# Performance work log

Measured on AMD Instinct MI355X. Metric: run time of the kernel, lower is better.

The kernel has to match this reference:

```python
import jax, jax.numpy as jnp
import numpy as np

NUM_EXPERTS = 64
TOP_K = 2


def setup_inputs() -> dict:
    key = jax.random.key(0)
    k1, k2 = jax.random.split(key)
    hidden_states = jax.random.normal(k1, (4, 8192, 2048), dtype=jnp.float32)
    # torch nn.Linear weight layout: (num_experts, hidden)
    W = jax.random.normal(k2, (NUM_EXPERTS, 2048), dtype=jnp.float32) * 0.02
    return {"hidden_states": hidden_states, "W": W}


def reference(hidden_states, W):
    b, s, h = hidden_states.shape
    x = hidden_states.reshape(-1, h)                      # (T, H), T = b*s
    logits = jnp.einsum('th,eh->te', x, W)                # (T, E) skinny gate GEMM
    # eval mode: no gaussian noise added
    top_vals, indices = jax.lax.top_k(logits, TOP_K)      # (T, K)
    gates = jax.nn.softmax(top_vals, axis=-1)
    gates = gates.reshape(b, s, TOP_K)
    indices = indices.reshape(b, s, TOP_K)
    # load-balance auxiliary loss (faithful to source, incl. probs>0 mask)
    probs = jax.nn.softmax(logits, axis=-1)               # (T, E)
    mean_probs = probs.mean(axis=0)                       # (E,)
    routing_probs = (probs > 0).astype(logits.dtype).mean(axis=0)  # (E,)
    load_balance_loss = NUM_EXPERTS * jnp.sum(mean_probs * routing_probs)
    return (gates, indices, load_balance_loss)
```

## Files before the change

kernel.cpp:

```cpp
#include <hip/hip_runtime.h>
#include <math.h>

#define H      2048
#define HV     512
#define E      64
#define MTOK   8
#define T_TOK  32768
#define GATES_OFF   0
#define IDX_OFF     65536
#define LOSS_OFF    131072

__global__ void transpose_w_kernel(const float* __restrict__ W, float* __restrict__ Wt) {
    int id = blockIdx.x * 256 + threadIdx.x;
    int e = id >> 11;
    int h = id & 2047;
    Wt[(h >> 2) * 256 + (e << 2) + (h & 3)] = W[id];
}

__global__ __launch_bounds__(256) void gate_main_kernel(
        const float* __restrict__ x,
        const float4* __restrict__ wt,
        float* __restrict__ out,
        float* __restrict__ accum)
{
    const int lane = threadIdx.x & 63;
    const int wave = threadIdx.x >> 6;
    const int gwave = blockIdx.x * 4 + wave;
    const int tokBase = __builtin_amdgcn_readfirstlane(gwave * MTOK);

    const float4* __restrict__ xq = (const float4*)x + (size_t)tokBase * HV;

    float acc[MTOK];
#pragma unroll
    for (int m = 0; m < MTOK; ++m) acc[m] = 0.f;

    for (int i = 0; i < HV; ++i) {
        float4 wv = wt[i * E + lane];
#pragma unroll
        for (int m = 0; m < MTOK; ++m) {
            float4 xv = xq[m * HV + i];
            acc[m] = fmaf(xv.x, wv.x, acc[m]);
            acc[m] = fmaf(xv.y, wv.y, acc[m]);
            acc[m] = fmaf(xv.z, wv.z, acc[m]);
            acc[m] = fmaf(xv.w, wv.w, acc[m]);
        }
    }

    float sumP = 0.f, cntP = 0.f;

#pragma unroll
    for (int m = 0; m < MTOK; ++m) {
        float v = acc[m];

        float vmax = v;
#pragma unroll
        for (int d = 32; d > 0; d >>= 1) vmax = fmaxf(vmax, __shfl_xor(vmax, d, 64));
        float ex = expf(v - vmax);
        float s = ex;
#pragma unroll
        for (int d = 32; d > 0; d >>= 1) s += __shfl_xor(s, d, 64);
        float p = ex / s;
        sumP += p;
        cntP += (p > 0.f) ? 1.f : 0.f;

        float v1 = v; int i1 = lane;
#pragma unroll
        for (int d = 32; d > 0; d >>= 1) {
            float ov = __shfl_xor(v1, d, 64);
            int   oi = __shfl_xor(i1, d, 64);
            if (ov > v1 || (ov == v1 && oi < i1)) { v1 = ov; i1 = oi; }
        }
        float v2 = (lane == i1) ? -INFINITY : v; int i2 = lane;
#pragma unroll
        for (int d = 32; d > 0; d >>= 1) {
            float ov = __shfl_xor(v2, d, 64);
            int   oi = __shfl_xor(i2, d, 64);
            if (ov > v2 || (ov == v2 && oi < i2)) { v2 = ov; i2 = oi; }
        }

        if (lane == 0) {
            int token = tokBase + m;
            float t  = expf(v2 - v1);
            float d  = 1.f / (1.f + t);
            out[GATES_OFF + 2 * token]     = d;
            out[GATES_OFF + 2 * token + 1] = t * d;
            out[IDX_OFF   + 2 * token]     = (float)i1;
            out[IDX_OFF   + 2 * token + 1] = (float)i2;
        }
    }

    __shared__ float redP[4][64];
    __shared__ float redC[4][64];
    redP[wave][lane] = sumP;
    redC[wave][lane] = cntP;
    __syncthreads();
    if (wave == 0) {
        float sp = redP[0][lane] + redP[1][lane] + redP[2][lane] + redP[3][lane];
        float sc = redC[0][lane] + redC[1][lane] + redC[2][lane] + redC[3][lane];
        atomicAdd(&accum[lane], sp);
        atomicAdd(&accum[E + lane], sc);
    }
}

__global__ void gate_final_kernel(const float* __restrict__ accum, float* __restrict__ out) {
    int lane = threadIdx.x;
    const float invT = 1.f / (float)T_TOK;
    float mean_p   = accum[lane] * invT;
    float routing  = accum[E + lane] * invT;
    float term = mean_p * routing;
#pragma unroll
    for (int d = 32; d > 0; d >>= 1) term += __shfl_xor(term, d, 64);
    if (lane == 0) out[LOSS_OFF] = 64.f * term;
}

extern "C" void kernel_launch(void* const* d_in, const int* in_sizes, int n_in,
                              void* d_out, int out_size, void* d_ws, size_t ws_size,
                              hipStream_t stream) {
    const float* x = (const float*)d_in[0];
    const float* W = (const float*)d_in[1];
    float* out   = (float*)d_out;
    float* accum = (float*)d_ws;
    float* Wt    = (float*)d_ws + 128;

    hipMemsetAsync(accum, 0, 128 * sizeof(float), stream);
    transpose_w_kernel<<<512, 256, 0, stream>>>(W, Wt);
    gate_main_kernel<<<T_TOK / (MTOK * 4), 256, 0, stream>>>(x, (const float4*)Wt, out, accum);
    gate_final_kernel<<<1, 64, 0, stream>>>(accum, out);
}
```

Measured before the change: 706.1 us.

## Stage x tiles into LDS with async global_load_lds double buffering

The main gate GEMM now stages 64-token by 64-element chunks of x into a double-buffered LDS tile using async global-to-LDS loads, so the next chunk streams in while the current one is computed. Each wave handles 16 tokens instead of 8, which reuses each W load across more tokens. Before, every lane read x per-token through scalar-uniform global loads. The accumulator memset is folded into the transpose kernel to drop one launch. In exchange the kernel pays a __syncthreads per chunk and more registers per thread. It also issues only 512 blocks, which may leave the GPU underoccupied.

```diff
diff --git a/kernel.cpp b/kernel.cpp
--- a/kernel.cpp
+++ b/kernel.cpp
@@ -2,51 +2,91 @@
 #include <math.h>
 
 #define H      2048
-#define HV     512
 #define E      64
-#define MTOK   8
+#define MTOK   16
+#define BTOK   64
+#define KC     64
+#define KC4    16
+#define NCHUNK (H / KC)
 #define T_TOK  32768
 #define GATES_OFF   0
 #define IDX_OFF     65536
 #define LOSS_OFF    131072
 
-__global__ void transpose_w_kernel(const float* __restrict__ W, float* __restrict__ Wt) {
+__global__ void transpose_w_kernel(const float* __restrict__ W, float* __restrict__ Wt,
+                                   float* __restrict__ accum) {
     int id = blockIdx.x * 256 + threadIdx.x;
+    if (blockIdx.x == 0 && threadIdx.x < 128) accum[threadIdx.x] = 0.f;
     int e = id >> 11;
     int h = id & 2047;
     Wt[(h >> 2) * 256 + (e << 2) + (h & 3)] = W[id];
 }
 
+__device__ __forceinline__ void async_copy16(const float* g, void* l) {
+    __builtin_amdgcn_global_load_lds(
+        (const __attribute__((address_space(1))) unsigned int*)g,
+        (__attribute__((address_space(3))) unsigned int*)l,
+        16, 0, 0);
+}
+
 __global__ __launch_bounds__(256) void gate_main_kernel(
         const float* __restrict__ x,
-        const float4* __restrict__ wt,
+        const float4* __restrict__ wt4,
         float* __restrict__ out,
         float* __restrict__ accum)
 {
-    const int lane = threadIdx.x & 63;
-    const int wave = threadIdx.x >> 6;
-    const int gwave = blockIdx.x * 4 + wave;
-    const int tokBase = __builtin_amdgcn_readfirstlane(gwave * MTOK);
+    __shared__ float4 xtile[2][BTOK * KC4];
+    __shared__ float  redP[4][64];
+    __shared__ float  redC[4][64];
 
-    const float4* __restrict__ xq = (const float4*)x + (size_t)tokBase * HV;
+    const int tid  = threadIdx.x;
+    const int lane = tid & 63;
+    const int wave = tid >> 6;
+    const int tokBase = blockIdx.x * BTOK;
+
+    const float* xg = x + (size_t)tokBase * H;
+
+    auto stage = [&](int c, int b) {
+#pragma unroll
+        for (int j = 0; j < 4; ++j) {
+            int f = tid + j * 256;
+            int token = f >> 4;
+            int k4 = f & 15;
+            async_copy16(xg + (size_t)token * H + c * KC + k4 * 4, &xtile[b][f]);
+        }
+    };
 
     float acc[MTOK];
 #pragma unroll
     for (int m = 0; m < MTOK; ++m) acc[m] = 0.f;
 
-    for (int i = 0; i < HV; ++i) {
-        float4 wv = wt[i * E + lane];
+    stage(0, 0);
+
+    for (int c = 0; c < NCHUNK; ++c) {
+        const int b = c & 1;
+        __syncthreads();
+        if (c + 1 < NCHUNK) stage(c + 1, b ^ 1);
+
+        const float4* xw = &xtile[b][wave * (MTOK * KC4)];
+        const float4* wp = wt4 + (size_t)c * (KC4 * E) + lane;
 #pragma unroll
-        for (int m = 0; m < MTOK; ++m) {
-            float4 xv = xq[m * HV + i];
-            acc[m] = fmaf(xv.x, wv.x, acc[m]);
-            acc[m] = fmaf(xv.y, wv.y, acc[m]);
-            acc[m] = fmaf(xv.z, wv.z, acc[m]);
-            acc[m] = fmaf(xv.w, wv.w, acc[m]);
+        for (int k4 = 0; k4 < KC4; ++k4) {
+            float4 wv = wp[k4 * E];
+#pragma unroll
+            for (int m = 0; m < MTOK; ++m) {
+                float4 xv = xw[m * KC4 + k4];
+                float a = acc[m];
+                a = fmaf(xv.x, wv.x, a);
+                a = fmaf(xv.y, wv.y, a);
+                a = fmaf(xv.z, wv.z, a);
+                a = fmaf(xv.w, wv.w, a);
+                acc[m] = a;
+            }
         }
     }
 
     float sumP = 0.f, cntP = 0.f;
+    const int tokW = tokBase + wave * MTOK;
 
 #pragma unroll
     for (int m = 0; m < MTOK; ++m) {
@@ -79,7 +119,7 @@
         }
 
         if (lane == 0) {
-            int token = tokBase + m;
+            int token = tokW + m;
             float t  = expf(v2 - v1);
             float d  = 1.f / (1.f + t);
             out[GATES_OFF + 2 * token]     = d;
@@ -89,8 +129,6 @@
         }
     }
 
-    __shared__ float redP[4][64];
-    __shared__ float redC[4][64];
     redP[wave][lane] = sumP;
     redC[wave][lane] = cntP;
     __syncthreads();
@@ -122,8 +160,7 @@
     float* accum = (float*)d_ws;
     float* Wt    = (float*)d_ws + 128;
 
-    hipMemsetAsync(accum, 0, 128 * sizeof(float), stream);
-    transpose_w_kernel<<<512, 256, 0, stream>>>(W, Wt);
-    gate_main_kernel<<<T_TOK / (MTOK * 4), 256, 0, stream>>>(x, (const float4*)Wt, out, accum);
+    transpose_w_kernel<<<512, 256, 0, stream>>>(W, Wt, accum);
+    gate_main_kernel<<<T_TOK / BTOK, 256, 0, stream>>>(x, (const float4*)Wt, out, accum);
     gate_final_kernel<<<1, 64, 0, stream>>>(accum, out);
 }
```

Result: faster. 584.8 us (-17.2%).

## Restructure gate GEMM: lane-per-token, split-K across waves, LDS-staged X tiles

Applied to the files above, without the earlier changes.

Each block now handles 64 tokens, with each lane owning one token and accumulating all 64 expert logits in registers. The four waves split the hidden dimension and combine their partial sums through LDS. X tiles are staged into double-buffered, swizzled LDS with register prefetch, and W is read as wave-uniform broadcasts. This is meant to replace the per-lane redundant X loads of the old scheme with better reuse. The softmax/top-2 epilogue is reorganised into 4 lanes per token, and the accumulator memset is folded into the transpose kernel. The risk is higher register pressure from 64 accumulators, which may lower occupancy.

```diff
diff --git a/kernel.cpp b/kernel.cpp
--- a/kernel.cpp
+++ b/kernel.cpp
@@ -2,111 +2,190 @@
 #include <math.h>
 
 #define H      2048
-#define HV     512
+#define HV4    512
 #define E      64
-#define MTOK   8
 #define T_TOK  32768
+#define KS4    128
+#define KC4    8
+#define NCH    16
 #define GATES_OFF   0
 #define IDX_OFF     65536
 #define LOSS_OFF    131072
 
-__global__ void transpose_w_kernel(const float* __restrict__ W, float* __restrict__ Wt) {
+__global__ void transpose_w_kernel(const float* __restrict__ W, float* __restrict__ Wt,
+                                   float* __restrict__ accum) {
     int id = blockIdx.x * 256 + threadIdx.x;
+    if (blockIdx.x == 0 && threadIdx.x < 128) accum[threadIdx.x] = 0.f;
     int e = id >> 11;
     int h = id & 2047;
     Wt[(h >> 2) * 256 + (e << 2) + (h & 3)] = W[id];
 }
 
 __global__ __launch_bounds__(256) void gate_main_kernel(
-        const float* __restrict__ x,
-        const float4* __restrict__ wt,
+        const float4* __restrict__ x4,
+        const float4* __restrict__ wt4,
         float* __restrict__ out,
         float* __restrict__ accum)
 {
-    const int lane = threadIdx.x & 63;
-    const int wave = threadIdx.x >> 6;
-    const int gwave = blockIdx.x * 4 + wave;
-    const int tokBase = __builtin_amdgcn_readfirstlane(gwave * MTOK);
-
-    const float4* __restrict__ xq = (const float4*)x + (size_t)tokBase * HV;
-
-    float acc[MTOK];
-#pragma unroll
-    for (int m = 0; m < MTOK; ++m) acc[m] = 0.f;
-
-    for (int i = 0; i < HV; ++i) {
-        float4 wv = wt[i * E + lane];
-#pragma unroll
-        for (int m = 0; m < MTOK; ++m) {
-            float4 xv = xq[m * HV + i];
-            acc[m] = fmaf(xv.x, wv.x, acc[m]);
-            acc[m] = fmaf(xv.y, wv.y, acc[m]);
-            acc[m] = fmaf(xv.z, wv.z, acc[m]);
-            acc[m] = fmaf(xv.w, wv.w, acc[m]);
-        }
-    }
-
-    float sumP = 0.f, cntP = 0.f;
-
-#pragma unroll
-    for (int m = 0; m < MTOK; ++m) {
-        float v = acc[m];
-
-        float vmax = v;
-#pragma unroll
-        for (int d = 32; d > 0; d >>= 1) vmax = fmaxf(vmax, __shfl_xor(vmax, d, 64));
-        float ex = expf(v - vmax);
-        float s = ex;
-#pragma unroll
-        for (int d = 32; d > 0; d >>= 1) s += __shfl_xor(s, d, 64);
-        float p = ex / s;
-        sumP += p;
-        cntP += (p > 0.f) ? 1.f : 0.f;
-
-        float v1 = v; int i1 = lane;
-#pragma unroll
-        for (int d = 32; d > 0; d >>= 1) {
-            float ov = __shfl_xor(v1, d, 64);
-            int   oi = __shfl_xor(i1, d, 64);
-            if (ov > v1 || (ov == v1 && oi < i1)) { v1 = ov; i1 = oi; }
-        }
-        float v2 = (lane == i1) ? -INFINITY : v; int i2 = lane;
-#pragma unroll
-        for (int d = 32; d > 0; d >>= 1) {
-            float ov = __shfl_xor(v2, d, 64);
-            int   oi = __shfl_xor(i2, d, 64);
-            if (ov > v2 || (ov == v2 && oi < i2)) { v2 = ov; i2 = oi; }
-        }
-
-        if (lane == 0) {
-            int token = tokBase + m;
-            float t  = expf(v2 - v1);
-            float d  = 1.f / (1.f + t);
-            out[GATES_OFF + 2 * token]     = d;
-            out[GATES_OFF + 2 * token + 1] = t * d;
-            out[IDX_OFF   + 2 * token]     = (float)i1;
-            out[IDX_OFF   + 2 * token + 1] = (float)i2;
-        }
-    }
-
-    __shared__ float redP[4][64];
-    __shared__ float redC[4][64];
-    redP[wave][lane] = sumP;
-    redC[wave][lane] = cntP;
+    __shared__ float4 lds[4096];
+
+    const int tid  = threadIdx.x;
+    const int lane = tid & 63;
+    const int w    = __builtin_amdgcn_readfirstlane(tid >> 6);
+    const int tokBase = blockIdx.x * 64;
+    const int kbase4  = w * KS4;
+
+    float acc[E];
+#pragma unroll
+    for (int e = 0; e < E; ++e) acc[e] = 0.f;
+
+    float4* xt = &lds[w * 1024];
+
+    const int stok = lane >> 3;
+    const int sk4  = lane & 7;
+
+    float4 xbuf[8];
+
+    auto g_load = [&](int c) {
+#pragma unroll
+        for (int j = 0; j < 8; ++j) {
+            int tok = j * 8 + stok;
+            xbuf[j] = x4[(size_t)(tokBase + tok) * HV4 + kbase4 + c * KC4 + sk4];
+        }
+    };
+    auto l_store = [&](int c) {
+        float4* dst = xt + (c & 1) * 512;
+#pragma unroll
+        for (int j = 0; j < 8; ++j) {
+            int tok = j * 8 + stok;
+            dst[tok * 8 + (sk4 ^ (tok & 7))] = xbuf[j];
+        }
+    };
+
+    auto compute = [&](int c) {
+        const float4* src = xt + (c & 1) * 512 + lane * 8;
+        const int swz = lane & 7;
+        const float4* wrow = wt4 + (size_t)(kbase4 + c * KC4) * E;
+#pragma unroll 2
+        for (int k4 = 0; k4 < KC4; ++k4) {
+            float4 xv = src[k4 ^ swz];
+            const float4* wp = wrow + k4 * E;
+#pragma unroll
+            for (int e = 0; e < E; ++e) {
+                float4 wv = wp[e];
+                acc[e] = fmaf(xv.x, wv.x, acc[e]);
+                acc[e] = fmaf(xv.y, wv.y, acc[e]);
+                acc[e] = fmaf(xv.z, wv.z, acc[e]);
+                acc[e] = fmaf(xv.w, wv.w, acc[e]);
+            }
+        }
+    };
+
+    g_load(0);
+    l_store(0);
+    for (int c = 0; c < NCH; ++c) {
+        if (c + 1 < NCH) g_load(c + 1);
+        compute(c);
+        if (c + 1 < NCH) l_store(c + 1);
+    }
+
     __syncthreads();
-    if (wave == 0) {
-        float sp = redP[0][lane] + redP[1][lane] + redP[2][lane] + redP[3][lane];
-        float sc = redC[0][lane] + redC[1][lane] + redC[2][lane] + redC[3][lane];
-        atomicAdd(&accum[lane], sp);
-        atomicAdd(&accum[E + lane], sc);
+    float4* P = lds;
+    {
+        float4* dst = &P[(w * 64 + lane) * 16];
+#pragma unroll
+        for (int e4 = 0; e4 < 16; ++e4)
+            dst[e4] = make_float4(acc[4*e4], acc[4*e4+1], acc[4*e4+2], acc[4*e4+3]);
+    }
+    __syncthreads();
+
+    const int tl  = lane >> 2;
+    const int eq  = lane & 3;
+    const int tok = tokBase + w * 16 + tl;
+    const int prow = w * 16 + tl;
+
+    float l16[16];
+#pragma unroll
+    for (int j4 = 0; j4 < 4; ++j4) {
+        float4 s0 = P[(0 * 64 + prow) * 16 + eq * 4 + j4];
+        float4 s1 = P[(1 * 64 + prow) * 16 + eq * 4 + j4];
+        float4 s2 = P[(2 * 64 + prow) * 16 + eq * 4 + j4];
+        float4 s3 = P[(3 * 64 + prow) * 16 + eq * 4 + j4];
+        l16[4*j4+0] = s0.x + s1.x + s2.x + s3.x;
+        l16[4*j4+1] = s0.y + s1.y + s2.y + s3.y;
+        l16[4*j4+2] = s0.z + s1.z + s2.z + s3.z;
+        l16[4*j4+3] = s0.w + s1.w + s2.w + s3.w;
+    }
+
+    float m = l16[0];
+#pragma unroll
+    for (int j = 1; j < 16; ++j) m = fmaxf(m, l16[j]);
+    m = fmaxf(m, __shfl_xor(m, 1));
+    m = fmaxf(m, __shfl_xor(m, 2));
+    float ex[16], ssum = 0.f;
+#pragma unroll
+    for (int j = 0; j < 16; ++j) { ex[j] = expf(l16[j] - m); ssum += ex[j]; }
+    ssum += __shfl_xor(ssum, 1);
+    ssum += __shfl_xor(ssum, 2);
+    const float inv = 1.f / ssum;
+
+    float sP[16], sC[16];
+#pragma unroll
+    for (int j = 0; j < 16; ++j) {
+        float p = ex[j] * inv;
+        sP[j] = p;
+        sC[j] = (p > 0.f) ? 1.f : 0.f;
+    }
+#pragma unroll
+    for (int j = 0; j < 16; ++j) {
+#pragma unroll
+        for (int d = 4; d <= 32; d <<= 1) {
+            sP[j] += __shfl_xor(sP[j], d);
+            sC[j] += __shfl_xor(sC[j], d);
+        }
+    }
+    if (lane < 4) {
+#pragma unroll
+        for (int j = 0; j < 16; ++j) {
+            atomicAdd(&accum[eq * 16 + j], sP[j]);
+            atomicAdd(&accum[E + eq * 16 + j], sC[j]);
+        }
+    }
+
+    float v1 = l16[0]; int i1 = eq * 16;
+    float v2 = -INFINITY; int i2 = -1;
+#pragma unroll
+    for (int j = 1; j < 16; ++j) {
+        float v = l16[j]; int e = eq * 16 + j;
+        if (v > v1)      { v2 = v1; i2 = i1; v1 = v; i1 = e; }
+        else if (v > v2) { v2 = v; i2 = e; }
+    }
+#pragma unroll
+    for (int d = 1; d <= 2; d <<= 1) {
+        float bv1 = __shfl_down(v1, d); int bi1 = __shfl_down(i1, d);
+        float bv2 = __shfl_down(v2, d); int bi2 = __shfl_down(i2, d);
+        if (bv1 > v1) {
+            if (bv2 > v1) { v2 = bv2; i2 = bi2; } else { v2 = v1; i2 = i1; }
+            v1 = bv1; i1 = bi1;
+        } else {
+            if (bv1 > v2) { v2 = bv1; i2 = bi1; }
+        }
+    }
+    if (eq == 0) {
+        float t  = expf(v2 - v1);
+        float g1 = 1.f / (1.f + t);
+        out[GATES_OFF + 2 * tok]     = g1;
+        out[GATES_OFF + 2 * tok + 1] = t * g1;
+        out[IDX_OFF   + 2 * tok]     = (float)i1;
+        out[IDX_OFF   + 2 * tok + 1] = (float)i2;
     }
 }
 
 __global__ void gate_final_kernel(const float* __restrict__ accum, float* __restrict__ out) {
     int lane = threadIdx.x;
     const float invT = 1.f / (float)T_TOK;
-    float mean_p   = accum[lane] * invT;
-    float routing  = accum[E + lane] * invT;
+    float mean_p  = accum[lane] * invT;
+    float routing = accum[E + lane] * invT;
     float term = mean_p * routing;
 #pragma unroll
     for (int d = 32; d > 0; d >>= 1) term += __shfl_xor(term, d, 64);
@@ -122,8 +201,7 @@
     float* accum = (float*)d_ws;
     float* Wt    = (float*)d_ws + 128;
 
-    hipMemsetAsync(accum, 0, 128 * sizeof(float), stream);
-    transpose_w_kernel<<<512, 256, 0, stream>>>(W, Wt);
-    gate_main_kernel<<<T_TOK / (MTOK * 4), 256, 0, stream>>>(x, (const float4*)Wt, out, accum);
+    transpose_w_kernel<<<512, 256, 0, stream>>>(W, Wt, accum);
+    gate_main_kernel<<<T_TOK / 64, 256, 0, stream>>>((const float4*)x, (const float4*)Wt, out, accum);
     gate_final_kernel<<<1, 64, 0, stream>>>(accum, out);
 }
```

Result: slower. 1.355 ms (+91.9%).
